# Performance work log

Measured on AMD Instinct MI355X. Metric: run time of the kernel, lower is better.

The kernel has to match this reference:

```python
import jax, jax.numpy as jnp
import numpy as np

N, E, G = 50000, 800000, 64
DIMS = [(32, 4, 64), (256, 4, 128), (512, 4, 64)]
EPS = 1e-5  # BatchNorm eps (eval mode, running mean=0, var=1)


def setup_inputs():
    key = jax.random.key(0)
    ks = list(jax.random.split(key, 40))
    it = iter(range(40))
    nxt = lambda: ks[next(it)]
    inp = {}
    inp['x'] = jax.random.normal(nxt(), (N, 32), jnp.float32)
    inp['edge_feature'] = jax.random.normal(nxt(), (E, 6), jnp.float32)
    for li, (fin, H, C) in enumerate(DIMS, 1):
        s = 1.0 / np.sqrt(fin).astype(np.float32)
        inp[f'W{li}'] = jax.random.normal(nxt(), (fin, H * C), jnp.float32) * s
        inp[f'We{li}'] = jax.random.normal(nxt(), (6, H * C), jnp.float32) * 0.3
        inp[f'as{li}'] = jax.random.normal(nxt(), (H, C), jnp.float32) * 0.1
        inp[f'ad{li}'] = jax.random.normal(nxt(), (H, C), jnp.float32) * 0.1
        inp[f'ae{li}'] = jax.random.normal(nxt(), (H, C), jnp.float32) * 0.1
        inp[f'b{li}'] = jnp.zeros((H * C,), jnp.float32)
        inp[f'g{li}'] = jnp.ones((H * C,), jnp.float32)
        inp[f'bb{li}'] = jnp.zeros((H * C,), jnp.float32)
    inp['Wf1'] = jax.random.normal(nxt(), (256, 32), jnp.float32) * 0.0625
    inp['bf1'] = jnp.zeros((32,), jnp.float32)
    inp['gf'] = jnp.ones((32,), jnp.float32)
    inp['bbf'] = jnp.zeros((32,), jnp.float32)
    inp['Wf2'] = jax.random.normal(nxt(), (32, 2), jnp.float32) * 0.2
    inp['bf2'] = jnp.zeros((2,), jnp.float32)
    inp['edge_index'] = jax.random.randint(nxt(), (2, E), 0, N)
    inp['batch'] = jnp.sort(jax.random.randint(nxt(), (N,), 0, G))
    return inp


def _bn(h, g, b):
    # eval-mode BatchNorm1d with running mean 0, running var 1
    return g * h * (1.0 / jnp.sqrt(1.0 + EPS)) + b


def _gat(h, ea, src, dst, W, We, a_s, a_d, a_e, b):
    H, C = a_s.shape
    xs = (h @ W).reshape(N, H, C)                       # shared lin for src/dst
    al_s = jnp.einsum('nhc,hc->nh', xs, a_s)
    al_d = jnp.einsum('nhc,hc->nh', xs, a_d)
    al_e = jnp.einsum('ehc,hc->eh', (ea @ We).reshape(-1, H, C), a_e)
    al = jax.nn.leaky_relu(al_s[src] + al_d[dst] + al_e, 0.2)  # [E+N, H]
    m = jax.ops.segment_max(al, dst, num_segments=N)
    w = jnp.exp(al - m[dst])
    w = w / (jax.ops.segment_sum(w, dst, num_segments=N)[dst] + 1e-16)
    out = jax.ops.segment_sum(xs[src] * w[:, :, None], dst, num_segments=N)
    return out.reshape(N, H * C) + b


def _forward(x, edge_feature, W1, We1, as1, ad1, ae1, b1, g1, bb1,
             W2, We2, as2, ad2, ae2, b2, g2, bb2,
             W3, We3, as3, ad3, ae3, b3, g3, bb3,
             Wf1, bf1, gf, bbf, Wf2, bf2, edge_index, batch):
    src0, dst0 = edge_index[0], edge_index[1]
    # add self loops; self-loop edge_attr = per-dst mean (PyG fill_value='mean')
    deg = jax.ops.segment_sum(jnp.ones((E,), x.dtype), dst0, num_segments=N)
    emean = jax.ops.segment_sum(edge_feature, dst0, num_segments=N) / jnp.maximum(deg, 1.0)[:, None]
    loops = jnp.arange(N)
    src = jnp.concatenate([src0, loops])
    dst = jnp.concatenate([dst0, loops])
    ea = jnp.concatenate([edge_feature, emean], axis=0)
    h = jax.nn.elu(_bn(_gat(x, ea, src, dst, W1, We1, as1, ad1, ae1, b1), g1, bb1))
    h = jax.nn.elu(_bn(_gat(h, ea, src, dst, W2, We2, as2, ad2, ae2, b2), g2, bb2))
    h = jax.nn.elu(_bn(_gat(h, ea, src, dst, W3, We3, as3, ad3, ae3, b3), g3, bb3))
    cnt = jax.ops.segment_sum(jnp.ones((N,), h.dtype), batch, num_segments=G)
    pooled = jax.ops.segment_sum(h, batch, num_segments=G) / jnp.maximum(cnt, 1.0)[:, None]
    h = jax.nn.elu(_bn(pooled @ Wf1 + bf1, gf, bbf))
    return jax.nn.log_softmax(h @ Wf2 + bf2, axis=1)


def reference(x, edge_feature, W1, We1, as1, ad1, ae1, b1, g1, bb1,
              W2, We2, as2, ad2, ae2, b2, g2, bb2,
              W3, We3, as3, ad3, ae3, b3, g3, bb3,
              Wf1, bf1, gf, bbf, Wf2, bf2, edge_index, batch):
    return _forward(x, edge_feature, W1, We1, as1, ad1, ae1, b1, g1, bb1,
                    W2, We2, as2, ad2, ae2, b2, g2, bb2,
                    W3, We3, as3, ad3, ae3, b3, g3, bb3,
                    Wf1, bf1, gf, bbf, Wf2, bf2, edge_index, batch)
```

## Files before the change

### kernel.cpp

```cpp
#include <hip/hip_runtime.h>
#include <cstdint>
#include <cstddef>

#define NN 50000
#define NPAD 50048
#define EE 800000
#define ET (EE + NN)
#define GG 64
#define HH 4
#define RSQ 0.9999950000374997f

typedef short bf16x8 __attribute__((ext_vector_type(8)));
typedef unsigned short u16x8 __attribute__((ext_vector_type(8)));
typedef float f32x4 __attribute__((ext_vector_type(4)));
typedef float f32x2 __attribute__((ext_vector_type(2)));

__device__ __forceinline__ float bf2f(unsigned short u) {
    union { unsigned int i; float f; } v; v.i = ((unsigned int)u) << 16; return v.f;
}
__device__ __forceinline__ unsigned short f2bf(float f) {
    union { float f; unsigned int i; } v; v.f = f;
    unsigned int u = v.i;
    u += 0x7fffu + ((u >> 16) & 1u);
    return (unsigned short)(u >> 16);
}


#if __has_builtin(__builtin_amdgcn_cvt_pk_fp8_f32) && __has_builtin(__builtin_amdgcn_cvt_pk_f32_fp8)
#define FP8_HW 1
#else
#define FP8_HW 0
#endif

#if !FP8_HW
__device__ __forceinline__ unsigned int enc1_fp8(float f) {
    unsigned int u = __float_as_uint(f);
    unsigned int s = (u >> 24) & 0x80u;
    float a = fabsf(f);
    a = fminf(a, 448.f);
    unsigned int b;
    if (a >= 0.015625f) {
        unsigned int ub = __float_as_uint(a);
        unsigned int mant = ub & 0x7FFFFFu;
        unsigned int keep = mant >> 20;
        unsigned int rem = mant & 0xFFFFFu;
        unsigned int exp = (ub >> 23) - 127u + 7u;
        unsigned int q = (exp << 3) | keep;
        if (rem > 0x80000u || (rem == 0x80000u && (q & 1u))) q++;
        if (q > 0x7Eu) q = 0x7Eu;
        b = q;
    } else {
        int q = (int)(a * 512.0f + 0.5f);
        b = (q > 7) ? 0x08u : (unsigned int)q;
    }
    return s | b;
}
__device__ __forceinline__ float dec1_fp8(unsigned int b) {
    unsigned int sgn = (b & 0x80u) << 24;
    float r;
    if (b & 0x78u) {
        r = __uint_as_float(sgn | (((b & 0x7Fu) + 0x3C0u) << 20));
    } else {
        r = (float)(b & 7u) * 0x1p-9f;
        r = (b & 0x80u) ? -r : r;
    }
    return r;
}
#endif

__device__ __forceinline__ unsigned int pk4_fp8(float f0, float f1, float f2, float f3) {
#if FP8_HW
    int r = __builtin_amdgcn_cvt_pk_fp8_f32(f0, f1, 0, false);
    r = __builtin_amdgcn_cvt_pk_fp8_f32(f2, f3, r, true);
    return (unsigned int)r;
#else
    return enc1_fp8(f0) | (enc1_fp8(f1) << 8) | (enc1_fp8(f2) << 16) | (enc1_fp8(f3) << 24);
#endif
}

__device__ __forceinline__ f32x2 dec2lo_fp8(unsigned int u) {
#if FP8_HW
    return __builtin_amdgcn_cvt_pk_f32_fp8((int)u, false);
#else
    f32x2 r; r[0] = dec1_fp8(u & 0xFFu); r[1] = dec1_fp8((u >> 8) & 0xFFu); return r;
#endif
}
__device__ __forceinline__ f32x2 dec2hi_fp8(unsigned int u) {
#if FP8_HW
    return __builtin_amdgcn_cvt_pk_f32_fp8((int)u, true);
#else
    f32x2 r; r[0] = dec1_fp8((u >> 16) & 0xFFu); r[1] = dec1_fp8(u >> 24); return r;
#endif
}

static inline void* carve(char*& p, size_t bytes) {
    void* r = (void*)p;
    p += (bytes + 255) & ~(size_t)255;
    return r;
}


__global__ void deg_kernel(const int* __restrict__ dst0, int* __restrict__ deg,
                           int* __restrict__ epos) {
    int e = blockIdx.x * blockDim.x + threadIdx.x;
    if (e >= EE) return;
    epos[e] = atomicAdd(&deg[dst0[e]], 1);
}

#define SCAN_B 512
__global__ void scan1_kernel(const int* __restrict__ deg, int* __restrict__ out,
                             int* __restrict__ bsum, int n) {
    __shared__ int tmp[SCAN_B];
    int i = blockIdx.x * SCAN_B + threadIdx.x;
    int v = (i < n) ? (deg[i] + 1) : 0;
    tmp[threadIdx.x] = v;
    __syncthreads();
    for (int off = 1; off < SCAN_B; off <<= 1) {
        int t = (threadIdx.x >= off) ? tmp[threadIdx.x - off] : 0;
        __syncthreads();
        tmp[threadIdx.x] += t;
        __syncthreads();
    }
    if (i < n) out[i] = tmp[threadIdx.x] - v;
    if (threadIdx.x == SCAN_B - 1) bsum[blockIdx.x] = tmp[threadIdx.x];
}

__global__ void scan2_kernel(int* __restrict__ bsum, int nb) {
    __shared__ int tmp[128];
    int v = (threadIdx.x < nb) ? bsum[threadIdx.x] : 0;
    tmp[threadIdx.x] = v;
    __syncthreads();
    for (int off = 1; off < 128; off <<= 1) {
        int t = (threadIdx.x >= off) ? tmp[threadIdx.x - off] : 0;
        __syncthreads();
        tmp[threadIdx.x] += t;
        __syncthreads();
    }
    if (threadIdx.x < nb) bsum[threadIdx.x] = tmp[threadIdx.x] - v;
}

__global__ void scan3_kernel(int* __restrict__ out, const int* __restrict__ bsum, int n) {
    int i = blockIdx.x * SCAN_B + threadIdx.x;
    if (i < n) out[i] += bsum[blockIdx.x];
    if (i == 0 && blockIdx.x == 0) out[n] = ET;
}

__global__ void fill_kernel(const int* __restrict__ src0, const int* __restrict__ dst0,
                            const int* __restrict__ row_ptr, const int* __restrict__ epos,
                            const int* __restrict__ deg,
                            int* __restrict__ ssrc, int* __restrict__ seid) {
    int e = blockIdx.x * blockDim.x + threadIdx.x;
    if (e < EE) {
        int idx = row_ptr[dst0[e]] + epos[e];
        ssrc[idx] = src0[e];
        seid[idx] = e;
    } else if (e < ET) {
        int n = e - EE;
        int idx = row_ptr[n] + deg[n];
        ssrc[idx] = n;
        seid[idx] = EE + n;
    }
}


__global__ void convx_kernel(const float* __restrict__ x, unsigned short* __restrict__ xb) {
    int i = blockIdx.x * blockDim.x + threadIdx.x;
    if (i >= NPAD * 64) return;
    int row = i >> 6, col = i & 63;
    float v = 0.f;
    if (row < NN && col < 32) v = x[(size_t)row * 32 + col];
    xb[i] = f2bf(v);
}

__global__ void convw_all_kernel(const float* __restrict__ W1, const float* __restrict__ W2,
                                 const float* __restrict__ W3,
                                 unsigned short* __restrict__ Wt1,
                                 unsigned short* __restrict__ Wt2,
                                 unsigned short* __restrict__ Wt3) {
    int i = blockIdx.x * blockDim.x + threadIdx.x;
    if (i < 16384) {
        int c = i >> 6, k = i & 63;
        Wt1[i] = (k < 32) ? f2bf(W1[(size_t)k * 256 + c]) : (unsigned short)0;
    } else if (i < 16384 + 131072) {
        int j = i - 16384;
        int c = j >> 8, k = j & 255;
        Wt2[j] = f2bf(W2[(size_t)k * 512 + c]);
    } else if (i < 16384 + 262144) {
        int j = i - 147456;
        int c = j >> 9, k = j & 511;
        Wt3[j] = f2bf(W3[(size_t)k * 256 + c]);
    }
}

__global__ void wea_all_kernel(const float* __restrict__ We1, const float* __restrict__ ae1,
                               const float* __restrict__ We2, const float* __restrict__ ae2,
                               const float* __restrict__ We3, const float* __restrict__ ae3,
                               float* __restrict__ Wea) {
    int t = threadIdx.x;
    if (t >= 72) return;
    int l = t / 24, w = t % 24, k = w / 4, h = w % 4;
    const float* We = (l == 0) ? We1 : (l == 1) ? We2 : We3;
    const float* ae = (l == 0) ? ae1 : (l == 1) ? ae2 : ae3;
    int C = (l == 1) ? 128 : 64;
    int HC = 4 * C;
    float s = 0.f;
    for (int c = 0; c < C; c++) s += We[(size_t)k * HC + h * C + c] * ae[(size_t)h * C + c];
    Wea[l * 24 + k * 4 + h] = s;
}


#if __has_builtin(__builtin_amdgcn_global_load_lds)
#define GLL_OK 1
#else
#define GLL_OK 0
#endif

#define TILE_LD 136

template <int C_>
__global__ __launch_bounds__(256) void gemm_fused_kernel(const unsigned short* __restrict__ A,
                                                         const unsigned short* __restrict__ Bt,
                                                         unsigned char* __restrict__ X8,
                                                         const float* __restrict__ a_s,
                                                         const float* __restrict__ a_d,
                                                         float* __restrict__ als,
                                                         float* __restrict__ ald,
                                                         int K) {
    constexpr int HC = HH * C_;
    __shared__ unsigned short smem[128 * TILE_LD + 64];
    unsigned short* As = smem;
    unsigned short* Bs = smem + 8192;
    const int tid = threadIdx.x;
    const int bm = blockIdx.x * 128;
    const int bn = blockIdx.y * 128;
    const int lane = tid & 63;
    const int wv = tid >> 6;
    const int wrow = (wv >> 1) * 64;
    const int wcol = (wv & 1) * 64;
    const int l15 = lane & 15;
    const int q = lane >> 4;

    f32x4 acc[4][4];
#pragma unroll
    for (int m = 0; m < 4; m++)
#pragma unroll
        for (int n = 0; n < 4; n++) acc[m][n] = (f32x4)0.f;

    for (int k0 = 0; k0 < K; k0 += 64) {
#pragma unroll
        for (int i = 0; i < 4; i++) {
            int c = (wv * 4 + i) * 64 + lane;
            int row = c >> 3, slot = c & 7;
            int slotG = slot ^ (row & 7);
            const unsigned short* ga = &A[(size_t)(bm + row) * K + k0 + slotG * 8];
            const unsigned short* gb = &Bt[(size_t)(bn + row) * K + k0 + slotG * 8];
#if GLL_OK
            __builtin_amdgcn_global_load_lds(
                (const __attribute__((address_space(1))) unsigned int*)ga,
                (__attribute__((address_space(3))) unsigned int*)&As[(size_t)(wv * 4 + i) * 512],
                16, 0, 0);
            __builtin_amdgcn_global_load_lds(
                (const __attribute__((address_space(1))) unsigned int*)gb,
                (__attribute__((address_space(3))) unsigned int*)&Bs[(size_t)(wv * 4 + i) * 512],
                16, 0, 0);
#else
            *(u16x8*)&As[(size_t)c * 8] = *(const u16x8*)ga;
            *(u16x8*)&Bs[(size_t)c * 8] = *(const u16x8*)gb;
#endif
        }
        __syncthreads();
#pragma unroll
        for (int kk = 0; kk < 2; kk++) {
            bf16x8 af[4], bfr[4];
#pragma unroll
            for (int m = 0; m < 4; m++) {
                int ra = wrow + m * 16 + l15;
                af[m] = *(const bf16x8*)&As[ra * 64 + ((kk * 4 + q) ^ (ra & 7)) * 8];
            }
#pragma unroll
            for (int n = 0; n < 4; n++) {
                int rb = wcol + n * 16 + l15;
                bfr[n] = *(const bf16x8*)&Bs[rb * 64 + ((kk * 4 + q) ^ (rb & 7)) * 8];
            }
#pragma unroll
            for (int m = 0; m < 4; m++)
#pragma unroll
                for (int n = 0; n < 4; n++)
                    acc[m][n] = __builtin_amdgcn_mfma_f32_16x16x32_bf16(af[m], bfr[n], acc[m][n], 0, 0, 0);
        }
        __syncthreads();
    }

    unsigned short* tile = smem;
#pragma unroll
    for (int m = 0; m < 4; m++) {
#pragma unroll
        for (int n = 0; n < 4; n++) {
#pragma unroll
            for (int j = 0; j < 4; j++) {
                int r = wrow + m * 16 + (lane >> 4) * 4 + j;
                int c = wcol + n * 16 + l15;
                tile[r * TILE_LD + c] = f2bf(acc[m][n][j]);
            }
        }
    }
    __syncthreads();

    const int tcol = tid & 15;
    const int trow = tid >> 4;
    float as8[8], ad8[8];
#pragma unroll
    for (int k = 0; k < 8; k++) {
        as8[k] = a_s[bn + tcol * 8 + k];
        ad8[k] = a_d[bn + tcol * 8 + k];
    }
#pragma unroll
    for (int i = 0; i < 8; i++) {
        int r = i * 16 + trow;
        int grow = bm + r;
        u16x8 v = *(const u16x8*)&tile[r * TILE_LD + tcol * 8];
        float f[8];
#pragma unroll
        for (int k = 0; k < 8; k++) f[k] = bf2f(v[k]);
        unsigned int r0 = pk4_fp8(f[0], f[1], f[2], f[3]);
        unsigned int r1 = pk4_fp8(f[4], f[5], f[6], f[7]);
        *(uint2*)&X8[(size_t)grow * HC + bn + tcol * 8] = make_uint2(r0, r1);
        float ps = 0.f, pd = 0.f;
#pragma unroll
        for (int k = 0; k < 8; k++) { ps += f[k] * as8[k]; pd += f[k] * ad8[k]; }
        if constexpr (C_ == 64) {
            ps += __shfl_xor(ps, 1); pd += __shfl_xor(pd, 1);
            ps += __shfl_xor(ps, 2); pd += __shfl_xor(pd, 2);
            ps += __shfl_xor(ps, 4); pd += __shfl_xor(pd, 4);
            if ((tid & 7) == 0 && grow < NN) {
                int head = (bn >> 6) + (tcol >> 3);
                als[(size_t)grow * HH + head] = ps;
                ald[(size_t)grow * HH + head] = pd;
            }
        } else {
            ps += __shfl_xor(ps, 1); pd += __shfl_xor(pd, 1);
            ps += __shfl_xor(ps, 2); pd += __shfl_xor(pd, 2);
            ps += __shfl_xor(ps, 4); pd += __shfl_xor(pd, 4);
            ps += __shfl_xor(ps, 8); pd += __shfl_xor(pd, 8);
            if ((tid & 15) == 0 && grow < NN) {
                int head = bn >> 7;
                als[(size_t)grow * HH + head] = ps;
                ald[(size_t)grow * HH + head] = pd;
            }
        }
    }
}


template <int C_>
__global__ __launch_bounds__(256) void aggregate_fused_kernel(
        const unsigned char* __restrict__ xs8,
        const int* __restrict__ rowptr, const int* __restrict__ ssrc,
        const int* __restrict__ seid, const float* __restrict__ ef,
        const float* __restrict__ Wea,
        const float* __restrict__ als, const float* __restrict__ ald,
        float* __restrict__ al,
        const float* __restrict__ bias, const float* __restrict__ gam,
        const float* __restrict__ bet, unsigned short* __restrict__ hout) {
    constexpr int HC = HH * C_;
    constexpr int CPL = HC / 64;
    int wid = (blockIdx.x * blockDim.x + threadIdx.x) >> 6;
    int lane = threadIdx.x & 63;
    if (wid >= NN) return;
    int b = rowptr[wid], e = rowptr[wid + 1];
    int cnt = e - b;
    const int hpre = lane >> 4;
    const int m15 = lane & 15;
    float inv = 1.0f / fmaxf((float)(cnt - 1), 1.0f);
    float4 ad4 = *(const float4*)&ald[(size_t)wid * 4];

    f32x2 acc2[CPL / 2];
#pragma unroll
    for (int k = 0; k < CPL / 2; k++) acc2[k] = (f32x2)0.f;
    const unsigned char* xbase = xs8 + (size_t)lane * CPL;

    auto accum_window = [&](int spre, const float* wpre, int cnt8) {
        for (int j = 0; j < cnt8; j += 8) {
            if constexpr (CPL == 8) {
                uint2 pk[8];
                float ww[8];
#pragma unroll
                for (int u = 0; u < 8; u++) {
                    int jj = j + u;
                    int s = __shfl(spre, jj);
                    ww[u] = __shfl(wpre[jj >> 4], (hpre << 4) | (jj & 15));
                    pk[u] = *(const uint2*)(xbase + (size_t)s * HC);
                }
#pragma unroll
                for (int u = 0; u < 8; u++) {
                    f32x2 wv; wv[0] = ww[u]; wv[1] = ww[u];
                    acc2[0] += wv * dec2lo_fp8(pk[u].x);
                    acc2[1] += wv * dec2hi_fp8(pk[u].x);
                    acc2[2] += wv * dec2lo_fp8(pk[u].y);
                    acc2[3] += wv * dec2hi_fp8(pk[u].y);
                }
            } else {
                unsigned int pk[8];
                float ww[8];
#pragma unroll
                for (int u = 0; u < 8; u++) {
                    int jj = j + u;
                    int s = __shfl(spre, jj);
                    ww[u] = __shfl(wpre[jj >> 4], (hpre << 4) | (jj & 15));
                    pk[u] = *(const unsigned int*)(xbase + (size_t)s * HC);
                }
#pragma unroll
                for (int u = 0; u < 8; u++) {
                    f32x2 wv; wv[0] = ww[u]; wv[1] = ww[u];
                    acc2[0] += wv * dec2lo_fp8(pk[u]);
                    acc2[1] += wv * dec2hi_fp8(pk[u]);
                }
            }
        }
    };

    if (cnt <= 64) {
        bool has = (lane < cnt);
        int i = b + lane;
        int eid = has ? seid[i] : EE;
        int s = has ? ssrc[i] : wid;
        float ev[6] = {0.f, 0.f, 0.f, 0.f, 0.f, 0.f};
        if (has && eid < EE) {
            const float* ep = &ef[(size_t)eid * 6];
#pragma unroll
            for (int k = 0; k < 6; k++) ev[k] = ep[k];
        }
        float es[6];
#pragma unroll
        for (int k = 0; k < 6; k++) es[k] = ev[k];
#pragma unroll
        for (int off = 32; off; off >>= 1)
#pragma unroll
            for (int k = 0; k < 6; k++) es[k] += __shfl_xor(es[k], off);
        if (has && eid >= EE) {
#pragma unroll
            for (int k = 0; k < 6; k++) ev[k] = es[k] * inv;
        }
        float4 as4 = make_float4(0.f, 0.f, 0.f, 0.f);
        if (has) as4 = *(const float4*)&als[(size_t)s * 4];
        float o[4] = {as4.x + ad4.x, as4.y + ad4.y, as4.z + ad4.z, as4.w + ad4.w};
#pragma unroll
        for (int h = 0; h < 4; h++) {
#pragma unroll
            for (int k = 0; k < 6; k++) o[h] += ev[k] * Wea[k * 4 + h];
            o[h] = o[h] > 0.f ? o[h] : 0.2f * o[h];
        }
        float m0 = has ? o[0] : -1e30f, m1 = has ? o[1] : -1e30f;
        float m2 = has ? o[2] : -1e30f, m3 = has ? o[3] : -1e30f;
#pragma unroll
        for (int off = 32; off; off >>= 1) {
            m0 = fmaxf(m0, __shfl_xor(m0, off)); m1 = fmaxf(m1, __shfl_xor(m1, off));
            m2 = fmaxf(m2, __shfl_xor(m2, off)); m3 = fmaxf(m3, __shfl_xor(m3, off));
        }
        float w4[4];
        w4[0] = has ? __expf(o[0] - m0) : 0.f;
        w4[1] = has ? __expf(o[1] - m1) : 0.f;
        w4[2] = has ? __expf(o[2] - m2) : 0.f;
        w4[3] = has ? __expf(o[3] - m3) : 0.f;
        float s0 = w4[0], s1 = w4[1], s2 = w4[2], s3 = w4[3];
#pragma unroll
        for (int off = 32; off; off >>= 1) {
            s0 += __shfl_xor(s0, off); s1 += __shfl_xor(s1, off);
            s2 += __shfl_xor(s2, off); s3 += __shfl_xor(s3, off);
        }
        w4[0] *= 1.f / (s0 + 1e-16f); w4[1] *= 1.f / (s1 + 1e-16f);
        w4[2] *= 1.f / (s2 + 1e-16f); w4[3] *= 1.f / (s3 + 1e-16f);
        float wpre[4];
#pragma unroll
        for (int q = 0; q < 4; q++) {
            int srcl = q * 16 + m15;
            float t0 = __shfl(w4[0], srcl), t1 = __shfl(w4[1], srcl);
            float t2 = __shfl(w4[2], srcl), t3 = __shfl(w4[3], srcl);
            wpre[q] = (hpre == 0) ? t0 : (hpre == 1) ? t1 : (hpre == 2) ? t2 : t3;
        }
        accum_window(s, wpre, (cnt + 7) & ~7);
    } else {
        float es[6] = {0.f, 0.f, 0.f, 0.f, 0.f, 0.f};
        for (int i = b + lane; i < e; i += 64) {
            int eid = seid[i];
            if (eid < EE) {
                const float* ep = &ef[(size_t)eid * 6];
#pragma unroll
                for (int k = 0; k < 6; k++) es[k] += ep[k];
            }
        }
#pragma unroll
        for (int off = 32; off; off >>= 1)
#pragma unroll
            for (int k = 0; k < 6; k++) es[k] += __shfl_xor(es[k], off);
        float em[6];
#pragma unroll
        for (int k = 0; k < 6; k++) em[k] = es[k] * inv;

        float m0 = -1e30f, m1 = -1e30f, m2 = -1e30f, m3 = -1e30f;
        for (int i = b + lane; i < e; i += 64) {
            int eid = seid[i];
            int s = ssrc[i];
            float4 as4 = *(const float4*)&als[(size_t)s * 4];
            float ev[6];
            if (eid < EE) {
                const float* ep = &ef[(size_t)eid * 6];
#pragma unroll
                for (int k = 0; k < 6; k++) ev[k] = ep[k];
            } else {
#pragma unroll
                for (int k = 0; k < 6; k++) ev[k] = em[k];
            }
            float o[4] = {as4.x + ad4.x, as4.y + ad4.y, as4.z + ad4.z, as4.w + ad4.w};
#pragma unroll
            for (int h = 0; h < 4; h++) {
#pragma unroll
                for (int k = 0; k < 6; k++) o[h] += ev[k] * Wea[k * 4 + h];
                o[h] = o[h] > 0.f ? o[h] : 0.2f * o[h];
            }
            *(float4*)&al[(size_t)i * 4] = make_float4(o[0], o[1], o[2], o[3]);
            m0 = fmaxf(m0, o[0]); m1 = fmaxf(m1, o[1]);
            m2 = fmaxf(m2, o[2]); m3 = fmaxf(m3, o[3]);
        }
#pragma unroll
        for (int off = 32; off; off >>= 1) {
            m0 = fmaxf(m0, __shfl_xor(m0, off)); m1 = fmaxf(m1, __shfl_xor(m1, off));
            m2 = fmaxf(m2, __shfl_xor(m2, off)); m3 = fmaxf(m3, __shfl_xor(m3, off));
        }
        float s0 = 0.f, s1 = 0.f, s2 = 0.f, s3 = 0.f;
        for (int i = b + lane; i < e; i += 64) {
            float4 v = *(const float4*)&al[(size_t)i * 4];
            s0 += __expf(v.x - m0); s1 += __expf(v.y - m1);
            s2 += __expf(v.z - m2); s3 += __expf(v.w - m3);
        }
#pragma unroll
        for (int off = 32; off; off >>= 1) {
            s0 += __shfl_xor(s0, off); s1 += __shfl_xor(s1, off);
            s2 += __shfl_xor(s2, off); s3 += __shfl_xor(s3, off);
        }
        float r0 = 1.f / (s0 + 1e-16f), r1 = 1.f / (s1 + 1e-16f);
        float r2 = 1.f / (s2 + 1e-16f), r3 = 1.f / (s3 + 1e-16f);
        float mh = (hpre == 0) ? m0 : (hpre == 1) ? m1 : (hpre == 2) ? m2 : m3;
        float rh = (hpre == 0) ? r0 : (hpre == 1) ? r1 : (hpre == 2) ? r2 : r3;

        for (int base = b; base < e; base += 64) {
            int c = e - base; if (c > 64) c = 64;
            int spre = (base + lane < e) ? ssrc[base + lane] : wid;
            float wpre[4];
#pragma unroll
            for (int q = 0; q < 4; q++) {
                int idx = base + q * 16 + m15;
                wpre[q] = (idx < e) ? __expf(al[(size_t)idx * 4 + hpre] - mh) * rh : 0.f;
            }
            accum_window(spre, wpre, (c + 7) & ~7);
        }
    }

    float acc[CPL];
#pragma unroll
    for (int k = 0; k < CPL / 2; k++) { acc[2 * k] = acc2[k][0]; acc[2 * k + 1] = acc2[k][1]; }
    int base_c = lane * CPL;
    unsigned int opk[CPL / 2];
#pragma unroll
    for (int q = 0; q < CPL / 4; q++) {
        float4 bi = *(const float4*)&bias[base_c + q * 4];
        float4 ga = *(const float4*)&gam[base_c + q * 4];
        float4 be = *(const float4*)&bet[base_c + q * 4];
        float vv[4];
        vv[0] = ga.x * (acc[q * 4 + 0] + bi.x) * RSQ + be.x;
        vv[1] = ga.y * (acc[q * 4 + 1] + bi.y) * RSQ + be.y;
        vv[2] = ga.z * (acc[q * 4 + 2] + bi.z) * RSQ + be.z;
        vv[3] = ga.w * (acc[q * 4 + 3] + bi.w) * RSQ + be.w;
#pragma unroll
        for (int k = 0; k < 4; k++) vv[k] = vv[k] > 0.f ? vv[k] : (__expf(vv[k]) - 1.0f);
        opk[q * 2 + 0] = (unsigned int)f2bf(vv[0]) | ((unsigned int)f2bf(vv[1]) << 16);
        opk[q * 2 + 1] = (unsigned int)f2bf(vv[2]) | ((unsigned int)f2bf(vv[3]) << 16);
    }
    if constexpr (CPL == 4) {
        *(uint2*)&hout[(size_t)wid * HC + base_c] = make_uint2(opk[0], opk[1]);
    } else {
        *(uint4*)&hout[(size_t)wid * HC + base_c] = make_uint4(opk[0], opk[1], opk[2], opk[3]);
    }
}


__global__ void bounds_kernel(const int* __restrict__ batch, int* __restrict__ first,
                              int* __restrict__ last) {
    int n = blockIdx.x * blockDim.x + threadIdx.x;
    if (n >= NN) return;
    int b = batch[n];
    if (n == 0 || batch[n - 1] != b) first[b] = n;
    if (n == NN - 1 || batch[n + 1] != b) last[b] = n;
}

#define PCHUNK 64
__global__ __launch_bounds__(256) void pool_kernel(const unsigned short* __restrict__ h3,
                                                   const int* __restrict__ batch,
                                                   float* __restrict__ pooled) {
    int c = threadIdx.x;
    int n0 = blockIdx.x * PCHUNK;
    int nend = min(n0 + PCHUNK, NN);
    if (n0 >= NN) return;
    float local = 0.f;
    int curg = batch[n0];
    for (int n = n0; n < nend; n++) {
        int g = batch[n];
        if (g != curg) {
            atomicAdd(&pooled[(size_t)curg * 256 + c], local);
            local = 0.f;
            curg = g;
        }
        local += bf2f(h3[(size_t)n * 256 + c]);
    }
    atomicAdd(&pooled[(size_t)curg * 256 + c], local);
}

__global__ void final_kernel(const float* __restrict__ pooled,
                             const int* __restrict__ first, const int* __restrict__ last,
                             const float* __restrict__ Wf1, const float* __restrict__ bf1,
                             const float* __restrict__ gf, const float* __restrict__ bbf,
                             const float* __restrict__ Wf2, const float* __restrict__ bf2,
                             float* __restrict__ out) {
    int g = blockIdx.x;
    int j = threadIdx.x;
    __shared__ float hh[32];
    float c = fmaxf((float)(last[g] - first[g] + 1), 1.0f);
    float inv = 1.0f / c;
    float acc = bf1[j];
    for (int i = 0; i < 256; i++) acc += (pooled[(size_t)g * 256 + i] * inv) * Wf1[(size_t)i * 32 + j];
    float v = gf[j] * acc * RSQ + bbf[j];
    hh[j] = v > 0.f ? v : (__expf(v) - 1.0f);
    __syncthreads();
    if (j == 0) {
        float l0 = bf2[0], l1 = bf2[1];
        for (int i = 0; i < 32; i++) {
            l0 += hh[i] * Wf2[i * 2 + 0];
            l1 += hh[i] * Wf2[i * 2 + 1];
        }
        float mx = fmaxf(l0, l1);
        float lse = mx + logf(__expf(l0 - mx) + __expf(l1 - mx));
        out[g * 2 + 0] = l0 - lse;
        out[g * 2 + 1] = l1 - lse;
    }
}


extern "C" void kernel_launch(void* const* d_in, const int* in_sizes, int n_in,
                              void* d_out, int out_size, void* d_ws, size_t ws_size,
                              hipStream_t stream) {
    (void)in_sizes; (void)n_in; (void)out_size; (void)ws_size;

    const float* x  = (const float*)d_in[0];
    const float* ef = (const float*)d_in[1];
    const float* W_[3]  = {(const float*)d_in[2],  (const float*)d_in[10], (const float*)d_in[18]};
    const float* We_[3] = {(const float*)d_in[3],  (const float*)d_in[11], (const float*)d_in[19]};
    const float* As_[3] = {(const float*)d_in[4],  (const float*)d_in[12], (const float*)d_in[20]};
    const float* Ad_[3] = {(const float*)d_in[5],  (const float*)d_in[13], (const float*)d_in[21]};
    const float* Ae_[3] = {(const float*)d_in[6],  (const float*)d_in[14], (const float*)d_in[22]};
    const float* Bi_[3] = {(const float*)d_in[7],  (const float*)d_in[15], (const float*)d_in[23]};
    const float* Ga_[3] = {(const float*)d_in[8],  (const float*)d_in[16], (const float*)d_in[24]};
    const float* Be_[3] = {(const float*)d_in[9],  (const float*)d_in[17], (const float*)d_in[25]};
    const float* Wf1 = (const float*)d_in[26];
    const float* bf1 = (const float*)d_in[27];
    const float* gf  = (const float*)d_in[28];
    const float* bbf = (const float*)d_in[29];
    const float* Wf2 = (const float*)d_in[30];
    const float* bf2 = (const float*)d_in[31];
    const int* eidx  = (const int*)d_in[32];
    const int* src0  = eidx;
    const int* dst0  = eidx + EE;
    const int* batch = (const int*)d_in[33];
    float* out = (float*)d_out;

    char* p = (char*)d_ws;
    unsigned short* B0 = (unsigned short*)carve(p, (size_t)NPAD * 512 * 2);
    unsigned short* B2 = (unsigned short*)carve(p, (size_t)NPAD * 512 * 2);
    unsigned char*  X8 = (unsigned char*)carve(p, (size_t)NPAD * 512);
    unsigned short* Wt1 = (unsigned short*)carve(p, (size_t)256 * 64 * 2);
    unsigned short* Wt2 = (unsigned short*)carve(p, (size_t)512 * 256 * 2);
    unsigned short* Wt3 = (unsigned short*)carve(p, (size_t)256 * 512 * 2);
    float* al     = (float*)carve(p, (size_t)ET * 4 * 4);
    float* als    = (float*)carve(p, (size_t)NN * 4 * 4);
    float* ald    = (float*)carve(p, (size_t)NN * 4 * 4);
    float* wea    = (float*)carve(p, 3 * 24 * 4);
    float* pooled = (float*)carve(p, (size_t)GG * 256 * 4);
    int* first  = (int*)carve(p, (size_t)GG * 4);
    int* last   = (int*)carve(p, (size_t)GG * 4);
    int* deg    = (int*)carve(p, (size_t)NN * 4);
    int* rowptr = (int*)carve(p, (size_t)(NN + 1) * 4);
    int* epos   = (int*)carve(p, (size_t)EE * 4);
    int* ssrc   = (int*)carve(p, (size_t)ET * 4);
    int* seid   = (int*)carve(p, (size_t)ET * 4);
    int* bsum   = (int*)carve(p, 512);

    hipMemsetAsync(deg, 0, (size_t)NN * 4, stream);
    hipMemsetAsync(pooled, 0, (size_t)GG * 256 * 4, stream);
    hipMemsetAsync(first, 0x00, (size_t)GG * 4, stream);
    hipMemsetAsync(last, 0xFF, (size_t)GG * 4, stream);

    deg_kernel<<<(EE + 255) / 256, 256, 0, stream>>>(dst0, deg, epos);

    int nb = (NN + SCAN_B - 1) / SCAN_B;
    scan1_kernel<<<nb, SCAN_B, 0, stream>>>(deg, rowptr, bsum, NN);
    scan2_kernel<<<1, 128, 0, stream>>>(bsum, nb);
    scan3_kernel<<<nb, SCAN_B, 0, stream>>>(rowptr, bsum, NN);
    fill_kernel<<<(ET + 255) / 256, 256, 0, stream>>>(src0, dst0, rowptr, epos, deg, ssrc, seid);

    convx_kernel<<<(NPAD * 64 + 255) / 256, 256, 0, stream>>>(x, B0);
    convw_all_kernel<<<(278528 + 255) / 256, 256, 0, stream>>>(W_[0], W_[1], W_[2], Wt1, Wt2, Wt3);
    wea_all_kernel<<<1, 128, 0, stream>>>(We_[0], Ae_[0], We_[1], Ae_[1], We_[2], Ae_[2], wea);

    int wblocks = (NN * 64 + 255) / 256;
    const int fpad[3] = {64, 256, 512};
    const int HCs[3] = {256, 512, 256};
    const int Cs[3]  = {64, 128, 64};
    const unsigned short* Wts[3] = {Wt1, Wt2, Wt3};
    const unsigned short* inb[3]  = {B0, B2, B0};
    unsigned short* outb[3]       = {B2, B0, B2};

    for (int li = 0; li < 3; li++) {
        int Kp = fpad[li], HC = HCs[li];
        dim3 gg(NPAD / 128, HC / 128);
        if (Cs[li] == 64)
            gemm_fused_kernel<64><<<gg, 256, 0, stream>>>(inb[li], Wts[li], X8,
                                                          As_[li], Ad_[li], als, ald, Kp);
        else
            gemm_fused_kernel<128><<<gg, 256, 0, stream>>>(inb[li], Wts[li], X8,
                                                           As_[li], Ad_[li], als, ald, Kp);

        if (Cs[li] == 64)
            aggregate_fused_kernel<64><<<wblocks, 256, 0, stream>>>(
                X8, rowptr, ssrc, seid, ef, wea + li * 24, als, ald, al,
                Bi_[li], Ga_[li], Be_[li], outb[li]);
        else
            aggregate_fused_kernel<128><<<wblocks, 256, 0, stream>>>(
                X8, rowptr, ssrc, seid, ef, wea + li * 24, als, ald, al,
                Bi_[li], Ga_[li], Be_[li], outb[li]);
    }

    bounds_kernel<<<(NN + 255) / 256, 256, 0, stream>>>(batch, first, last);
    pool_kernel<<<(NN + PCHUNK - 1) / PCHUNK, 256, 0, stream>>>(B2, batch, pooled);
    final_kernel<<<GG, 32, 0, stream>>>(pooled, first, last, Wf1, bf1, gf, bbf, Wf2, bf2, out);
}
```

Before: 451.9 us.

## Store edge features in CSR order and merge setup kernels

The fill kernel now copies each edge's 6 features into a CSR-ordered buffer, so the aggregation kernels read them contiguously instead of gathering through an edge-id indirection. Self-loop detection uses the row's last slot instead of the edge id. The four memsets become one zero kernel, and the x/weight conversion and Wea kernels are merged into a single prep kernel to cut launch count. The cost is an extra 20 MB buffer and a scattered write pass during fill.

```diff
diff --git a/kernel.cpp b/kernel.cpp
--- a/kernel.cpp
+++ b/kernel.cpp
@@ -100,6 +100,17 @@
 }
 
 
+__global__ void zero_kernel(int* __restrict__ deg, float* __restrict__ pooled,
+                            int* __restrict__ first, int* __restrict__ last) {
+    int i = blockIdx.x * blockDim.x + threadIdx.x;
+    if (i < NN) deg[i] = 0;
+    int j = i - NN;
+    if (j >= 0 && j < GG * 256) pooled[j] = 0.f;
+    int k = j - GG * 256;
+    if (k >= 0 && k < GG) { first[k] = 0; last[k] = -1; }
+}
+
+
 __global__ void deg_kernel(const int* __restrict__ dst0, int* __restrict__ deg,
                            int* __restrict__ epos) {
     int e = blockIdx.x * blockDim.x + threadIdx.x;
@@ -147,65 +158,74 @@
 
 __global__ void fill_kernel(const int* __restrict__ src0, const int* __restrict__ dst0,
                             const int* __restrict__ row_ptr, const int* __restrict__ epos,
-                            const int* __restrict__ deg,
-                            int* __restrict__ ssrc, int* __restrict__ seid) {
+                            const int* __restrict__ deg, const float* __restrict__ ef,
+                            int* __restrict__ ssrc, float* __restrict__ efc) {
     int e = blockIdx.x * blockDim.x + threadIdx.x;
     if (e < EE) {
         int idx = row_ptr[dst0[e]] + epos[e];
         ssrc[idx] = src0[e];
-        seid[idx] = e;
+        const float* s6 = &ef[(size_t)e * 6];
+        float* d6 = &efc[(size_t)idx * 6];
+        *(float2*)&d6[0] = *(const float2*)&s6[0];
+        *(float2*)&d6[2] = *(const float2*)&s6[2];
+        *(float2*)&d6[4] = *(const float2*)&s6[4];
     } else if (e < ET) {
         int n = e - EE;
         int idx = row_ptr[n] + deg[n];
         ssrc[idx] = n;
-        seid[idx] = EE + n;
-    }
-}
-
-
-__global__ void convx_kernel(const float* __restrict__ x, unsigned short* __restrict__ xb) {
+        float* d6 = &efc[(size_t)idx * 6];
+        float2 z = make_float2(0.f, 0.f);
+        *(float2*)&d6[0] = z; *(float2*)&d6[2] = z; *(float2*)&d6[4] = z;
+    }
+}
+
+
+#define PREP_X  (NPAD * 64)
+#define PREP_W1 (PREP_X + 16384)
+#define PREP_W2 (PREP_W1 + 131072)
+#define PREP_W3 (PREP_W2 + 131072)
+#define PREP_T  (PREP_W3 + 128)
+
+__global__ void prep_kernel(const float* __restrict__ x,
+                            const float* __restrict__ W1, const float* __restrict__ W2,
+                            const float* __restrict__ W3,
+                            const float* __restrict__ We1, const float* __restrict__ ae1,
+                            const float* __restrict__ We2, const float* __restrict__ ae2,
+                            const float* __restrict__ We3, const float* __restrict__ ae3,
+                            unsigned short* __restrict__ B0,
+                            unsigned short* __restrict__ Wt1, unsigned short* __restrict__ Wt2,
+                            unsigned short* __restrict__ Wt3, float* __restrict__ Wea) {
     int i = blockIdx.x * blockDim.x + threadIdx.x;
-    if (i >= NPAD * 64) return;
-    int row = i >> 6, col = i & 63;
-    float v = 0.f;
-    if (row < NN && col < 32) v = x[(size_t)row * 32 + col];
-    xb[i] = f2bf(v);
-}
-
-__global__ void convw_all_kernel(const float* __restrict__ W1, const float* __restrict__ W2,
-                                 const float* __restrict__ W3,
-                                 unsigned short* __restrict__ Wt1,
-                                 unsigned short* __restrict__ Wt2,
-                                 unsigned short* __restrict__ Wt3) {
-    int i = blockIdx.x * blockDim.x + threadIdx.x;
-    if (i < 16384) {
-        int c = i >> 6, k = i & 63;
-        Wt1[i] = (k < 32) ? f2bf(W1[(size_t)k * 256 + c]) : (unsigned short)0;
-    } else if (i < 16384 + 131072) {
-        int j = i - 16384;
+    if (i < PREP_X) {
+        int row = i >> 6, col = i & 63;
+        float v = 0.f;
+        if (row < NN && col < 32) v = x[(size_t)row * 32 + col];
+        B0[i] = f2bf(v);
+    } else if (i < PREP_W1) {
+        int j = i - PREP_X;
+        int c = j >> 6, k = j & 63;
+        Wt1[j] = (k < 32) ? f2bf(W1[(size_t)k * 256 + c]) : (unsigned short)0;
+    } else if (i < PREP_W2) {
+        int j = i - PREP_W1;
         int c = j >> 8, k = j & 255;
         Wt2[j] = f2bf(W2[(size_t)k * 512 + c]);
-    } else if (i < 16384 + 262144) {
-        int j = i - 147456;
+    } else if (i < PREP_W3) {
+        int j = i - PREP_W2;
         int c = j >> 9, k = j & 511;
         Wt3[j] = f2bf(W3[(size_t)k * 256 + c]);
-    }
-}
-
-__global__ void wea_all_kernel(const float* __restrict__ We1, const float* __restrict__ ae1,
-                               const float* __restrict__ We2, const float* __restrict__ ae2,
-                               const float* __restrict__ We3, const float* __restrict__ ae3,
-                               float* __restrict__ Wea) {
-    int t = threadIdx.x;
-    if (t >= 72) return;
-    int l = t / 24, w = t % 24, k = w / 4, h = w % 4;
-    const float* We = (l == 0) ? We1 : (l == 1) ? We2 : We3;
-    const float* ae = (l == 0) ? ae1 : (l == 1) ? ae2 : ae3;
-    int C = (l == 1) ? 128 : 64;
-    int HC = 4 * C;
-    float s = 0.f;
-    for (int c = 0; c < C; c++) s += We[(size_t)k * HC + h * C + c] * ae[(size_t)h * C + c];
-    Wea[l * 24 + k * 4 + h] = s;
+    } else if (i < PREP_T) {
+        int t = i - PREP_W3;
+        if (t < 72) {
+            int l = t / 24, w = t % 24, k = w / 4, h = w % 4;
+            const float* We = (l == 0) ? We1 : (l == 1) ? We2 : We3;
+            const float* ae = (l == 0) ? ae1 : (l == 1) ? ae2 : ae3;
+            int C = (l == 1) ? 128 : 64;
+            int HC = 4 * C;
+            float s = 0.f;
+            for (int c = 0; c < C; c++) s += We[(size_t)k * HC + h * C + c] * ae[(size_t)h * C + c];
+            Wea[l * 24 + k * 4 + h] = s;
+        }
+    }
 }
 
 
@@ -356,8 +376,7 @@
 __global__ __launch_bounds__(256) void aggregate_fused_kernel(
         const unsigned char* __restrict__ xs8,
         const int* __restrict__ rowptr, const int* __restrict__ ssrc,
-        const int* __restrict__ seid, const float* __restrict__ ef,
-        const float* __restrict__ Wea,
+        const float* __restrict__ efc, const float* __restrict__ Wea,
         const float* __restrict__ als, const float* __restrict__ ald,
         float* __restrict__ al,
         const float* __restrict__ bias, const float* __restrict__ gam,
@@ -421,14 +440,17 @@
 
     if (cnt <= 64) {
         bool has = (lane < cnt);
+        bool isself = (lane == cnt - 1);
         int i = b + lane;
-        int eid = has ? seid[i] : EE;
         int s = has ? ssrc[i] : wid;
         float ev[6] = {0.f, 0.f, 0.f, 0.f, 0.f, 0.f};
-        if (has && eid < EE) {
-            const float* ep = &ef[(size_t)eid * 6];
-#pragma unroll
-            for (int k = 0; k < 6; k++) ev[k] = ep[k];
+        if (has) {
+            const float* ep = &efc[(size_t)i * 6];
+            float2 a0 = *(const float2*)&ep[0];
+            float2 a1 = *(const float2*)&ep[2];
+            float2 a2 = *(const float2*)&ep[4];
+            ev[0] = a0.x; ev[1] = a0.y; ev[2] = a1.x;
+            ev[3] = a1.y; ev[4] = a2.x; ev[5] = a2.y;
         }
         float es[6];
 #pragma unroll
@@ -437,7 +459,7 @@
         for (int off = 32; off; off >>= 1)
 #pragma unroll
             for (int k = 0; k < 6; k++) es[k] += __shfl_xor(es[k], off);
-        if (has && eid >= EE) {
+        if (has && isself) {
 #pragma unroll
             for (int k = 0; k < 6; k++) ev[k] = es[k] * inv;
         }
@@ -482,12 +504,12 @@
     } else {
         float es[6] = {0.f, 0.f, 0.f, 0.f, 0.f, 0.f};
         for (int i = b + lane; i < e; i += 64) {
-            int eid = seid[i];
-            if (eid < EE) {
-                const float* ep = &ef[(size_t)eid * 6];
-#pragma unroll
-                for (int k = 0; k < 6; k++) es[k] += ep[k];
-            }
+            const float* ep = &efc[(size_t)i * 6];
+            float2 a0 = *(const float2*)&ep[0];
+            float2 a1 = *(const float2*)&ep[2];
+            float2 a2 = *(const float2*)&ep[4];
+            es[0] += a0.x; es[1] += a0.y; es[2] += a1.x;
+            es[3] += a1.y; es[4] += a2.x; es[5] += a2.y;
         }
 #pragma unroll
         for (int off = 32; off; off >>= 1)
@@ -499,14 +521,16 @@
 
         float m0 = -1e30f, m1 = -1e30f, m2 = -1e30f, m3 = -1e30f;
         for (int i = b + lane; i < e; i += 64) {
-            int eid = seid[i];
             int s = ssrc[i];
             float4 as4 = *(const float4*)&als[(size_t)s * 4];
             float ev[6];
-            if (eid < EE) {
-                const float* ep = &ef[(size_t)eid * 6];
-#pragma unroll
-                for (int k = 0; k < 6; k++) ev[k] = ep[k];
+            if (i != e - 1) {
+                const float* ep = &efc[(size_t)i * 6];
+                float2 a0 = *(const float2*)&ep[0];
+                float2 a1 = *(const float2*)&ep[2];
+                float2 a2 = *(const float2*)&ep[4];
+                ev[0] = a0.x; ev[1] = a0.y; ev[2] = a1.x;
+                ev[3] = a1.y; ev[4] = a2.x; ev[5] = a2.y;
             } else {
 #pragma unroll
                 for (int k = 0; k < 6; k++) ev[k] = em[k];
@@ -680,6 +704,7 @@
     unsigned short* Wt2 = (unsigned short*)carve(p, (size_t)512 * 256 * 2);
     unsigned short* Wt3 = (unsigned short*)carve(p, (size_t)256 * 512 * 2);
     float* al     = (float*)carve(p, (size_t)ET * 4 * 4);
+    float* efc    = (float*)carve(p, (size_t)ET * 6 * 4);
     float* als    = (float*)carve(p, (size_t)NN * 4 * 4);
     float* ald    = (float*)carve(p, (size_t)NN * 4 * 4);
     float* wea    = (float*)carve(p, 3 * 24 * 4);
@@ -690,13 +715,9 @@
     int* rowptr = (int*)carve(p, (size_t)(NN + 1) * 4);
     int* epos   = (int*)carve(p, (size_t)EE * 4);
     int* ssrc   = (int*)carve(p, (size_t)ET * 4);
-    int* seid   = (int*)carve(p, (size_t)ET * 4);
     int* bsum   = (int*)carve(p, 512);
 
-    hipMemsetAsync(deg, 0, (size_t)NN * 4, stream);
-    hipMemsetAsync(pooled, 0, (size_t)GG * 256 * 4, stream);
-    hipMemsetAsync(first, 0x00, (size_t)GG * 4, stream);
-    hipMemsetAsync(last, 0xFF, (size_t)GG * 4, stream);
+    zero_kernel<<<(NN + GG * 256 + 2 * GG + 255) / 256, 256, 0, stream>>>(deg, pooled, first, last);
 
     deg_kernel<<<(EE + 255) / 256, 256, 0, stream>>>(dst0, deg, epos);
 
@@ -704,11 +725,13 @@
     scan1_kernel<<<nb, SCAN_B, 0, stream>>>(deg, rowptr, bsum, NN);
     scan2_kernel<<<1, 128, 0, stream>>>(bsum, nb);
     scan3_kernel<<<nb, SCAN_B, 0, stream>>>(rowptr, bsum, NN);
-    fill_kernel<<<(ET + 255) / 256, 256, 0, stream>>>(src0, dst0, rowptr, epos, deg, ssrc, seid);
-
-    convx_kernel<<<(NPAD * 64 + 255) / 256, 256, 0, stream>>>(x, B0);
-    convw_all_kernel<<<(278528 + 255) / 256, 256, 0, stream>>>(W_[0], W_[1], W_[2], Wt1, Wt2, Wt3);
-    wea_all_kernel<<<1, 128, 0, stream>>>(We_[0], Ae_[0], We_[1], Ae_[1], We_[2], Ae_[2], wea);
+    fill_kernel<<<(ET + 255) / 256, 256, 0, stream>>>(src0, dst0, rowptr, epos, deg, ef,
+                                                      ssrc, efc);
+
+    prep_kernel<<<(PREP_T + 255) / 256, 256, 0, stream>>>(x, W_[0], W_[1], W_[2],
+                                                          We_[0], Ae_[0], We_[1], Ae_[1],
+                                                          We_[2], Ae_[2],
+                                                          B0, Wt1, Wt2, Wt3, wea);
 
     int wblocks = (NN * 64 + 255) / 256;
     const int fpad[3] = {64, 256, 512};
@@ -730,11 +753,11 @@
 
         if (Cs[li] == 64)
             aggregate_fused_kernel<64><<<wblocks, 256, 0, stream>>>(
-                X8, rowptr, ssrc, seid, ef, wea + li * 24, als, ald, al,
+                X8, rowptr, ssrc, efc, wea + li * 24, als, ald, al,
                 Bi_[li], Ga_[li], Be_[li], outb[li]);
         else
             aggregate_fused_kernel<128><<<wblocks, 256, 0, stream>>>(
-                X8, rowptr, ssrc, seid, ef, wea + li * 24, als, ald, al,
+                X8, rowptr, ssrc, efc, wea + li * 24, als, ald, al,
                 Bi_[li], Ga_[li], Be_[li], outb[li]);
     }
 
```

New measurement: 437.9 us. -3.1%, faster.
